# Optimization experiments

Hardware: AMD Instinct MI355X
Metric: run time of the kernel (lower is better)

## Reference

```python
import jax, jax.numpy as jnp
import numpy as np

B, CI, CO = 4, 64, 128
N_IN, N_OUT, K, P, H = 65536, 16384, 9, 4, 32
EPS = 1e-5


def setup_inputs() -> dict:
    key = jax.random.key(0)
    ks = jax.random.split(key, 16)
    inp = {
        "x": jax.random.normal(ks[0], (B, CI, N_IN), jnp.float32),
        "off1": jax.random.normal(ks[1], (N_OUT, K, 2), jnp.float32),
        "off2": jax.random.normal(ks[2], (N_OUT, K, 2), jnp.float32),
        "nbr1": jax.random.randint(ks[3], (N_OUT, K), 0, N_IN),
        "nbr2": jax.random.randint(ks[4], (N_OUT, K), 0, N_OUT),
        "pool_idx": jax.random.randint(ks[5], (N_OUT, P), 0, N_IN),
        # shared weight_net: 2 -> H -> 1 MLP producing per-neighbor interp weight
        "wn_w1": jax.random.normal(ks[6], (2, H), jnp.float32) * 0.5,
        "wn_b1": jnp.zeros((H,), jnp.float32),
        "wn_w2": jax.random.normal(ks[7], (H, 1), jnp.float32) * 0.5,
        "wn_b2": jnp.zeros((1,), jnp.float32),
        # conv weights [C_out, C_in, K]
        "W1": jax.random.normal(ks[8], (CO, CI, K), jnp.float32) * (1.0 / np.sqrt(CI * K)),
        "W2": jax.random.normal(ks[9], (CO, CO, K), jnp.float32) * (1.0 / np.sqrt(CO * K)),
        # batchnorm affine params
        "bn1_g": jnp.ones((CO,), jnp.float32),
        "bn1_b": jnp.zeros((CO,), jnp.float32),
        "bn2_g": jnp.ones((CO,), jnp.float32),
        "bn2_b": jnp.zeros((CO,), jnp.float32),
        # 1x1 expand conv
        "exp_w": jax.random.normal(ks[10], (CO, CI), jnp.float32) * (1.0 / np.sqrt(CI)),
        "exp_b": jnp.zeros((CO,), jnp.float32),
    }
    return inp


def _weight_net(off, w1, b1, w2, b2):
    # off: [M, K, 2] -> interp weights [M, K]
    h = jax.nn.relu(off @ w1 + b1)
    return (h @ w2 + b2)[..., 0]


def _interp_conv(x, W, idx, a):
    # x: [B, Ci, N_in], idx: [M, K], a: [M, K], W: [Co, Ci, K]
    g = x[:, :, idx]  # gather -> [B, Ci, M, K]
    return jnp.einsum("bimk,mk,oik->bom", g, a, W)


def _bn(x, g, b):
    # training-mode BatchNorm1d over (batch, points) per channel
    m = x.mean(axis=(0, 2), keepdims=True)
    v = x.var(axis=(0, 2), keepdims=True)
    return (x - m) * jax.lax.rsqrt(v + EPS) * g[None, :, None] + b[None, :, None]


def reference(x, off1, off2, wn_w1, wn_b1, wn_w2, wn_b2, W1, W2,
              bn1_g, bn1_b, bn2_g, bn2_b, exp_w, exp_b,
              nbr1, nbr2, pool_idx):
    a1 = _weight_net(off1, wn_w1, wn_b1, wn_w2, wn_b2)  # [M, K]
    out = _interp_conv(x, W1, nbr1, a1)                  # [B, Co, M]
    out = jax.nn.relu(_bn(out, bn1_g, bn1_b))
    a2 = _weight_net(off2, wn_w1, wn_b1, wn_w2, wn_b2)
    out = _interp_conv(out, W2, nbr2, a2)
    out = _bn(out, bn2_g, bn2_b)
    # downsample identity: AvgPoolNG over 4 nearest in_locs per out_loc
    identity = x[:, :, pool_idx].mean(axis=-1)           # [B, Ci, M]
    # expand channels: 1x1 conv
    identity = jnp.einsum("oi,bim->bom", exp_w, identity) + exp_b[None, :, None]
    return jax.nn.relu(out + identity)
```

## Files before the change

kernel.cpp:

```cpp
#include <hip/hip_runtime.h>
#include <hip/hip_bf16.h>

#define B_    4
#define CI_   64
#define CO_   128
#define NIN_  65536
#define NOUT_ 16384
#define KK_   9
#define PP_   4
#define HH_   32

typedef _Float16 f16x8 __attribute__((ext_vector_type(8)));
typedef _Float16 f16x4 __attribute__((ext_vector_type(4)));
typedef float    f32x4 __attribute__((ext_vector_type(4)));


__global__ void zero_kernel(float* p, int n) {
    int i = blockIdx.x * 256 + threadIdx.x;
    if (i < n) p[i] = 0.f;
}

__global__ void wnet_kernel(const float* __restrict__ off1, const float* __restrict__ off2,
                            const float* __restrict__ w1, const float* __restrict__ b1,
                            const float* __restrict__ w2, const float* __restrict__ b2,
                            float* __restrict__ a1, float* __restrict__ a2) {
    int idx = blockIdx.x * 256 + threadIdx.x;
    if (idx >= NOUT_ * KK_) return;
    float x0 = off1[idx*2+0], x1 = off1[idx*2+1];
    float y0 = off2[idx*2+0], y1 = off2[idx*2+1];
    float bias2 = b2[0];
    float s1 = bias2, s2 = bias2;
    #pragma unroll
    for (int h = 0; h < HH_; ++h) {
        float wh0 = w1[h], wh1 = w1[HH_+h], bh = b1[h], vh = w2[h];
        s1 += fmaxf(x0*wh0 + x1*wh1 + bh, 0.f) * vh;
        s2 += fmaxf(y0*wh0 + y1*wh1 + bh, 0.f) * vh;
    }
    a1[idx] = s1;
    a2[idx] = s2;
}

template<int CIN>
__global__ void wpack_kernel(const float* __restrict__ W, _Float16* __restrict__ Wf) {
    constexpr int NSLAB = (CIN/64) * KK_;
    int f = blockIdx.x * 256 + threadIdx.x;
    if (f >= NSLAB * 8192) return;
    int j   = f & 7;
    int l   = (f >> 3) & 63;
    int ot  = (f >> 9) & 7;
    int kap = (f >> 12) & 1;
    int s   = f >> 13;
    int o   = ot*16 + (l & 15);
    int kel = kap*32 + ((l >> 4) & 3)*8 + j;
    int k, i;
    if (CIN == 64) { k = s; i = kel; }
    else           { k = s >> 1; i = ((s & 1) << 6) + kel; }
    Wf[f] = (_Float16)W[((size_t)o*CIN + i)*KK_ + k];
}

__global__ void epack_kernel(const float* __restrict__ E, _Float16* __restrict__ Ef) {
    int f = blockIdx.x * 256 + threadIdx.x;
    if (f >= 8192) return;
    int j   = f & 7;
    int l   = (f >> 3) & 63;
    int ot  = (f >> 9) & 7;
    int kap = (f >> 12) & 1;
    int o   = ot*16 + (l & 15);
    int i   = kap*32 + ((l >> 4) & 3)*8 + j;
    Ef[f] = (_Float16)E[o*64 + i];
}

__global__ void xtrans_kernel(const float* __restrict__ x, _Float16* __restrict__ xT) {
    __shared__ float tile[64][65];
    int p0 = blockIdx.x * 64;
    int b  = blockIdx.y;
    int t  = threadIdx.x;
    #pragma unroll
    for (int r = 0; r < 16; ++r) {
        int f = r*256 + t;
        int i = f >> 6, pp = f & 63;
        tile[i][pp] = x[((size_t)(b*CI_ + i))*NIN_ + p0 + pp];
    }
    __syncthreads();
    #pragma unroll
    for (int r = 0; r < 2; ++r) {
        int f  = r*256 + t;
        int pp = f >> 3;
        int i0 = (f & 7) * 8;
        f16x8 v;
        #pragma unroll
        for (int e = 0; e < 8; ++e) v[e] = (_Float16)tile[i0+e][pp];
        *(f16x8*)(xT + ((size_t)(p0+pp)*B_ + b)*CI_ + i0) = v;
    }
}

__global__ __launch_bounds__(256) void bnreduce_kernel(const float* __restrict__ pbuf,
                                                       float* __restrict__ stats) {
    int t = threadIdx.x;
    float s = 0.f;
    int base = blockIdx.x * 32;
    #pragma unroll
    for (int b = 0; b < 32; ++b)
        s += pbuf[(size_t)(base + b)*256 + t];
    atomicAdd(&stats[t], s);
}

__global__ void bnparams_kernel(const float* __restrict__ gsum, const float* __restrict__ gsq,
                                const float* __restrict__ g, const float* __restrict__ bb,
                                const float* __restrict__ eb,
                                float* __restrict__ scbi) {
    int o = threadIdx.x;
    const float inv_n = 1.f / (B_ * NOUT_);
    float mean = gsum[o] * inv_n;
    float var  = gsq[o] * inv_n - mean*mean;
    float sc   = g[o] * rsqrtf(var + 1e-5f);
    scbi[o]       = sc;
    scbi[128 + o] = bb[o] - mean*sc + eb[o];
}

__global__ __launch_bounds__(256) void bnrelu_kernel(_Float16* __restrict__ t,
                                                     const float* __restrict__ scbi) {
    __shared__ float ssc[128], sbi[128];
    if (threadIdx.x < 128) {
        ssc[threadIdx.x] = scbi[threadIdx.x];
        sbi[threadIdx.x] = scbi[128 + threadIdx.x];
    }
    __syncthreads();
    size_t idx = ((size_t)blockIdx.x*256 + threadIdx.x) * 8;
    int o0 = (int)(idx & 127);
    f16x8 v = *(f16x8*)(t + idx);
    #pragma unroll
    for (int e = 0; e < 8; ++e) {
        float f = (float)v[e] * ssc[o0+e] + sbi[o0+e];
        v[e] = (_Float16)fmaxf(f, 0.f);
    }
    *(f16x8*)(t + idx) = v;
}

template<int CIN>
__global__ __launch_bounds__(256, CIN == 64 ? 4 : 3) void conv_mfma_kernel(
    const _Float16* __restrict__ in,
    const _Float16* __restrict__ Wf,
    const int*      __restrict__ nbr,
    const float*    __restrict__ amk,
    _Float16*       __restrict__ outh,
    float*          __restrict__ pbuf)
{
    constexpr int NKAP = CIN/32;
    __shared__ _Float16 Gs[2][64*CIN];
    const int t    = threadIdx.x;
    const int lane = t & 63;
    const int wid  = t >> 6;
    const int wr   = wid >> 1, wc = wid & 1;
    const int m0   = blockIdx.x * 16;
    const int l15 = lane & 15, l4 = lane >> 4, l7 = lane & 7;
    const int srow = t >> 2;
    const int sq   = t & 3;
    const int sb   = srow & 3;
    const int sm   = m0 + (srow >> 2);

    int   pn[KK_];
    float pa[KK_];
    #pragma unroll
    for (int k = 0; k < KK_; ++k) { pn[k] = nbr[sm*KK_ + k]; pa[k] = amk[sm*KK_ + k]; }

    f32x4 acc[4][2];
    #pragma unroll
    for (int c = 0; c < 4; ++c)
        #pragma unroll
        for (int j = 0; j < 2; ++j)
            acc[c][j] = (f32x4){0.f, 0.f, 0.f, 0.f};

    f16x8 greg[NKAP];
    {
        const _Float16* src = in + ((size_t)pn[0]*B_ + sb)*CIN + sq*(CIN/4);
        #pragma unroll
        for (int q = 0; q < NKAP; ++q) greg[q] = *(const f16x8*)(src + q*8);
    }

    #pragma unroll
    for (int s = 0; s < KK_; ++s) {
        const _Float16 hs = (_Float16)pa[s];
        #pragma unroll
        for (int q = 0; q < NKAP; ++q) {
            f16x8 v = greg[q];
            #pragma unroll
            for (int e = 0; e < 8; ++e) v[e] = v[e] * hs;
            const int c4 = sq*NKAP + q;
            *(f16x8*)(&Gs[s&1][srow*CIN + ((c4 ^ (srow & 7)) << 3)]) = v;
        }
        __syncthreads();
        f16x8 gn[NKAP];
        if (s + 1 < KK_) {
            const _Float16* src = in + ((size_t)pn[s+1]*B_ + sb)*CIN + sq*(CIN/4);
            #pragma unroll
            for (int q = 0; q < NKAP; ++q) gn[q] = *(const f16x8*)(src + q*8);
        }
        #pragma unroll
        for (int kap = 0; kap < NKAP; ++kap) {
            f16x8 aF[4], bF[2];
            const _Float16* wbase = Wf + ((size_t)(s*NKAP + kap)*8*64)*8;
            #pragma unroll
            for (int c = 0; c < 4; ++c)
                aF[c] = *(const f16x8*)(wbase + (((wr*4 + c)*64 + lane) << 3));
            #pragma unroll
            for (int jt = 0; jt < 2; ++jt) {
                const int row = wc*32 + jt*16 + l15;
                const int ch  = (kap*4 + l4) ^ l7;
                bF[jt] = *(const f16x8*)(&Gs[s&1][row*CIN + (ch << 3)]);
            }
            #pragma unroll
            for (int c = 0; c < 4; ++c)
                #pragma unroll
                for (int jt = 0; jt < 2; ++jt)
                    acc[c][jt] = __builtin_amdgcn_mfma_f32_16x16x32_f16(
                        aF[c], bF[jt], acc[c][jt], 0, 0, 0);
        }
        if (s + 1 < KK_) {
            #pragma unroll
            for (int q = 0; q < NKAP; ++q) greg[q] = gn[q];
        }
    }

    __syncthreads();
    float* red = (float*)Gs;
    #pragma unroll
    for (int c = 0; c < 4; ++c) {
        #pragma unroll
        for (int r = 0; r < 4; ++r) {
            float s = acc[c][0][r] + acc[c][1][r];
            float q = acc[c][0][r]*acc[c][0][r] + acc[c][1][r]*acc[c][1][r];
            #pragma unroll
            for (int msk = 1; msk <= 8; msk <<= 1) {
                s += __shfl_xor(s, msk);
                q += __shfl_xor(q, msk);
            }
            if (l15 == 0) {
                const int o = wr*64 + c*16 + l4*4 + r;
                red[wc*256 + o]       = s;
                red[wc*256 + 128 + o] = q;
            }
        }
    }
    __syncthreads();
    pbuf[(size_t)blockIdx.x*256 + t] = red[t] + red[256 + t];
    #pragma unroll
    for (int c = 0; c < 4; ++c) {
        const int o = wr*64 + c*16 + l4*4;
        #pragma unroll
        for (int jt = 0; jt < 2; ++jt) {
            const int n = wc*32 + jt*16 + l15;
            f16x4 h;
            #pragma unroll
            for (int r = 0; r < 4; ++r) h[r] = (_Float16)acc[c][jt][r];
            *(f16x4*)(outh + ((size_t)(m0*B_) + n)*CO_ + o) = h;
        }
    }
}

__global__ __launch_bounds__(256, 4) void final_mfma_kernel(
    const _Float16* __restrict__ xh,
    const _Float16* __restrict__ out2T,
    const int*      __restrict__ pool_idx,
    const _Float16* __restrict__ Ef,
    const float*    __restrict__ scbi2,
    float*          __restrict__ out)
{
    __shared__ _Float16 Gs[64*64];
    const int t    = threadIdx.x;
    const int lane = t & 63;
    const int wid  = t >> 6;
    const int wr   = wid >> 1, wc = wid & 1;
    const int m0   = blockIdx.x * 16;
    const int l15 = lane & 15, l4 = lane >> 4, l7 = lane & 7;

    {
        const int srow = t >> 2;
        const int sq   = t & 3;
        const int m    = m0 + (srow & 15);
        const int b    = srow >> 4;
        const int4 pidx = *(const int4*)(pool_idx + m*4);
        const _Float16* r0 = xh + ((size_t)pidx.x*B_ + b)*CI_ + sq*16;
        const _Float16* r1 = xh + ((size_t)pidx.y*B_ + b)*CI_ + sq*16;
        const _Float16* r2 = xh + ((size_t)pidx.z*B_ + b)*CI_ + sq*16;
        const _Float16* r3 = xh + ((size_t)pidx.w*B_ + b)*CI_ + sq*16;
        #pragma unroll
        for (int q = 0; q < 2; ++q) {
            f16x8 v  = *(const f16x8*)(r0 + q*8);
            f16x8 v1 = *(const f16x8*)(r1 + q*8);
            f16x8 v2 = *(const f16x8*)(r2 + q*8);
            f16x8 v3 = *(const f16x8*)(r3 + q*8);
            v = v + v1 + v2 + v3;
            #pragma unroll
            for (int e = 0; e < 8; ++e) v[e] = v[e] * (_Float16)0.25f;
            const int c4 = sq*2 + q;
            *(f16x8*)(Gs + srow*64 + ((c4 ^ (srow & 7)) << 3)) = v;
        }
    }
    __syncthreads();

    f32x4 acc[4][2];
    #pragma unroll
    for (int c = 0; c < 4; ++c)
        #pragma unroll
        for (int j = 0; j < 2; ++j)
            acc[c][j] = (f32x4){0.f, 0.f, 0.f, 0.f};
    #pragma unroll
    for (int kap = 0; kap < 2; ++kap) {
        f16x8 aF[4], bF[2];
        #pragma unroll
        for (int c = 0; c < 4; ++c)
            aF[c] = *(const f16x8*)(Ef + ((size_t)((kap*8 + wr*4 + c)*64 + lane))*8);
        #pragma unroll
        for (int jt = 0; jt < 2; ++jt) {
            const int row = wc*32 + jt*16 + l15;
            const int ch  = (kap*4 + l4) ^ l7;
            bF[jt] = *(const f16x8*)(Gs + row*64 + (ch << 3));
        }
        #pragma unroll
        for (int c = 0; c < 4; ++c)
            #pragma unroll
            for (int jt = 0; jt < 2; ++jt)
                acc[c][jt] = __builtin_amdgcn_mfma_f32_16x16x32_f16(
                    aF[c], bF[jt], acc[c][jt], 0, 0, 0);
    }

    const int m = m0 + l15;
    #pragma unroll
    for (int c = 0; c < 4; ++c) {
        const int o = wr*64 + c*16 + l4*4;
        const float4 sc4 = *(const float4*)(scbi2 + o);
        const float4 bi4 = *(const float4*)(scbi2 + 128 + o);
        #pragma unroll
        for (int jt = 0; jt < 2; ++jt) {
            const int b = wc*2 + jt;
            const f16x4 v2 = *(const f16x4*)(out2T + ((size_t)(m*B_ + b))*CO_ + o);
            float res0 = fmaxf(acc[c][jt][0] + (float)v2[0]*sc4.x + bi4.x, 0.f);
            float res1 = fmaxf(acc[c][jt][1] + (float)v2[1]*sc4.y + bi4.y, 0.f);
            float res2 = fmaxf(acc[c][jt][2] + (float)v2[2]*sc4.z + bi4.z, 0.f);
            float res3 = fmaxf(acc[c][jt][3] + (float)v2[3]*sc4.w + bi4.w, 0.f);
            out[((size_t)(b*CO_ + o + 0))*NOUT_ + m] = res0;
            out[((size_t)(b*CO_ + o + 1))*NOUT_ + m] = res1;
            out[((size_t)(b*CO_ + o + 2))*NOUT_ + m] = res2;
            out[((size_t)(b*CO_ + o + 3))*NOUT_ + m] = res3;
        }
    }
}

extern "C" void kernel_launch(void* const* d_in, const int* in_sizes, int n_in,
                              void* d_out, int out_size, void* d_ws, size_t ws_size,
                              hipStream_t stream) {
    const float* x        = (const float*)d_in[0];
    const float* off1     = (const float*)d_in[1];
    const float* off2     = (const float*)d_in[2];
    const int*   nbr1     = (const int*)  d_in[3];
    const int*   nbr2     = (const int*)  d_in[4];
    const int*   pool_idx = (const int*)  d_in[5];
    const float* wn_w1    = (const float*)d_in[6];
    const float* wn_b1    = (const float*)d_in[7];
    const float* wn_w2    = (const float*)d_in[8];
    const float* wn_b2    = (const float*)d_in[9];
    const float* W1       = (const float*)d_in[10];
    const float* W2       = (const float*)d_in[11];
    const float* bn1_g    = (const float*)d_in[12];
    const float* bn1_b    = (const float*)d_in[13];
    const float* bn2_g    = (const float*)d_in[14];
    const float* bn2_b    = (const float*)d_in[15];
    const float* exp_w    = (const float*)d_in[16];
    const float* exp_b    = (const float*)d_in[17];
    float* out = (float*)d_out;

    char* ws = (char*)d_ws;
    float* a1      = (float*)ws;  ws += (size_t)NOUT_*KK_*4;
    float* a2      = (float*)ws;  ws += (size_t)NOUT_*KK_*4;
    float* scbi1   = (float*)ws;  ws += 256*4;
    float* scbi2   = (float*)ws;  ws += 256*4;
    float* stats   = (float*)ws;  ws += 640*4;
    float* pbuf    = (float*)ws;  ws += (size_t)1024*256*4;
    _Float16* Wf1  = (_Float16*)ws; ws += (size_t)9*8192*2;
    _Float16* Wf2  = (_Float16*)ws; ws += (size_t)18*8192*2;
    _Float16* Ef   = (_Float16*)ws; ws += (size_t)8192*2;
    _Float16* xh   = (_Float16*)ws; ws += (size_t)NIN_*B_*CI_*2;
    _Float16* o1h  = (_Float16*)ws; ws += (size_t)NOUT_*B_*CO_*2;
    _Float16* o2h  = (_Float16*)ws; ws += (size_t)NOUT_*B_*CO_*2;

    float* sum1  = stats;       float* sq1 = stats + 128;
    float* sum2  = stats + 256; float* sq2 = stats + 384;
    float* fzero = stats + 512;

    zero_kernel<<<3, 256, 0, stream>>>(stats, 640);
    wnet_kernel<<<(NOUT_*KK_ + 255)/256, 256, 0, stream>>>(off1, off2, wn_w1, wn_b1, wn_w2, wn_b2, a1, a2);
    wpack_kernel<CI_><<<(9*8192 + 255)/256, 256, 0, stream>>>(W1, Wf1);
    wpack_kernel<CO_><<<(18*8192 + 255)/256, 256, 0, stream>>>(W2, Wf2);
    epack_kernel<<<32, 256, 0, stream>>>(exp_w, Ef);
    xtrans_kernel<<<dim3(NIN_/64, B_), 256, 0, stream>>>(x, xh);

    conv_mfma_kernel<CI_><<<NOUT_/16, 256, 0, stream>>>(xh, Wf1, nbr1, a1, o1h, pbuf);
    bnreduce_kernel<<<32, 256, 0, stream>>>(pbuf, sum1);
    bnparams_kernel<<<1, 128, 0, stream>>>(sum1, sq1, bn1_g, bn1_b, fzero, scbi1);
    bnrelu_kernel<<<4096, 256, 0, stream>>>(o1h, scbi1);

    conv_mfma_kernel<CO_><<<NOUT_/16, 256, 0, stream>>>(o1h, Wf2, nbr2, a2, o2h, pbuf);
    bnreduce_kernel<<<32, 256, 0, stream>>>(pbuf, sum2);
    bnparams_kernel<<<1, 128, 0, stream>>>(sum2, sq2, bn2_g, bn2_b, exp_b, scbi2);

    final_mfma_kernel<<<NOUT_/16, 256, 0, stream>>>(xh, o2h, pool_idx, Ef, scbi2, out);
}
```

Baseline: 132.6 us.

## Load conv B-fragments directly from global, dropping LDS staging and barriers

```diff
diff --git a/kernel.cpp b/kernel.cpp
--- a/kernel.cpp
+++ b/kernel.cpp
@@ -138,7 +138,7 @@
 }
 
 template<int CIN>
-__global__ __launch_bounds__(256, CIN == 64 ? 4 : 3) void conv_mfma_kernel(
+__global__ __launch_bounds__(256, 4) void conv_mfma_kernel(
     const _Float16* __restrict__ in,
     const _Float16* __restrict__ Wf,
     const int*      __restrict__ nbr,
@@ -147,22 +147,24 @@
     float*          __restrict__ pbuf)
 {
     constexpr int NKAP = CIN/32;
-    __shared__ _Float16 Gs[2][64*CIN];
+    constexpr int NST  = KK_ * NKAP;
+    __shared__ float red[512];
     const int t    = threadIdx.x;
     const int lane = t & 63;
     const int wid  = t >> 6;
     const int wr   = wid >> 1, wc = wid & 1;
+    const int wc2  = wc*2;
     const int m0   = blockIdx.x * 16;
-    const int l15 = lane & 15, l4 = lane >> 4, l7 = lane & 7;
-    const int srow = t >> 2;
-    const int sq   = t & 3;
-    const int sb   = srow & 3;
-    const int sm   = m0 + (srow >> 2);
-
-    int   pn[KK_];
-    float pa[KK_];
-    #pragma unroll
-    for (int k = 0; k < KK_; ++k) { pn[k] = nbr[sm*KK_ + k]; pa[k] = amk[sm*KK_ + k]; }
+    const int l15  = lane & 15, l4 = lane >> 4;
+
+    const int sm = m0 + l15;
+    int      pn[KK_];
+    _Float16 pa[KK_];
+    #pragma unroll
+    for (int k = 0; k < KK_; ++k) {
+        pn[k] = nbr[sm*KK_ + k];
+        pa[k] = (_Float16)amk[sm*KK_ + k];
+    }
 
     f32x4 acc[4][2];
     #pragma unroll
@@ -171,59 +173,40 @@
         for (int j = 0; j < 2; ++j)
             acc[c][j] = (f32x4){0.f, 0.f, 0.f, 0.f};
 
-    f16x8 greg[NKAP];
+    f16x8 bfr[2][2], afr[2][4];
     {
-        const _Float16* src = in + ((size_t)pn[0]*B_ + sb)*CIN + sq*(CIN/4);
-        #pragma unroll
-        for (int q = 0; q < NKAP; ++q) greg[q] = *(const f16x8*)(src + q*8);
-    }
-
-    #pragma unroll
-    for (int s = 0; s < KK_; ++s) {
-        const _Float16 hs = (_Float16)pa[s];
-        #pragma unroll
-        for (int q = 0; q < NKAP; ++q) {
-            f16x8 v = greg[q];
-            #pragma unroll
-            for (int e = 0; e < 8; ++e) v[e] = v[e] * hs;
-            const int c4 = sq*NKAP + q;
-            *(f16x8*)(&Gs[s&1][srow*CIN + ((c4 ^ (srow & 7)) << 3)]) = v;
-        }
-        __syncthreads();
-        f16x8 gn[NKAP];
-        if (s + 1 < KK_) {
-            const _Float16* src = in + ((size_t)pn[s+1]*B_ + sb)*CIN + sq*(CIN/4);
-            #pragma unroll
-            for (int q = 0; q < NKAP; ++q) gn[q] = *(const f16x8*)(src + q*8);
-        }
-        #pragma unroll
-        for (int kap = 0; kap < NKAP; ++kap) {
-            f16x8 aF[4], bF[2];
-            const _Float16* wbase = Wf + ((size_t)(s*NKAP + kap)*8*64)*8;
-            #pragma unroll
-            for (int c = 0; c < 4; ++c)
-                aF[c] = *(const f16x8*)(wbase + (((wr*4 + c)*64 + lane) << 3));
-            #pragma unroll
-            for (int jt = 0; jt < 2; ++jt) {
-                const int row = wc*32 + jt*16 + l15;
-                const int ch  = (kap*4 + l4) ^ l7;
-                bF[jt] = *(const f16x8*)(&Gs[s&1][row*CIN + (ch << 3)]);
-            }
-            #pragma unroll
-            for (int c = 0; c < 4; ++c)
-                #pragma unroll
-                for (int jt = 0; jt < 2; ++jt)
-                    acc[c][jt] = __builtin_amdgcn_mfma_f32_16x16x32_f16(
-                        aF[c], bF[jt], acc[c][jt], 0, 0, 0);
-        }
-        if (s + 1 < KK_) {
-            #pragma unroll
-            for (int q = 0; q < NKAP; ++q) greg[q] = gn[q];
-        }
-    }
-
-    __syncthreads();
-    float* red = (float*)Gs;
+        const _Float16* bsrc = in + ((size_t)pn[0]*B_ + wc2)*CIN + l4*8;
+        bfr[0][0] = *(const f16x8*)bsrc;
+        bfr[0][1] = *(const f16x8*)(bsrc + CIN);
+        const _Float16* wsrc = Wf + (size_t)(wr*4)*512 + lane*8;
+        #pragma unroll
+        for (int c = 0; c < 4; ++c) afr[0][c] = *(const f16x8*)(wsrc + c*512);
+    }
+
+    #pragma unroll
+    for (int st = 0; st < NST; ++st) {
+        const int cur = st & 1, nxt = cur ^ 1;
+        if (st + 1 < NST) {
+            const int s2 = (st+1) / NKAP, kap2 = (st+1) % NKAP;
+            const _Float16* bsrc = in + ((size_t)pn[s2]*B_ + wc2)*CIN + kap2*32 + l4*8;
+            bfr[nxt][0] = *(const f16x8*)bsrc;
+            bfr[nxt][1] = *(const f16x8*)(bsrc + CIN);
+            const _Float16* wsrc = Wf + ((size_t)((s2*NKAP + kap2)*8 + wr*4))*512 + lane*8;
+            #pragma unroll
+            for (int c = 0; c < 4; ++c) afr[nxt][c] = *(const f16x8*)(wsrc + c*512);
+        }
+        const int s = st / NKAP;
+        const _Float16 hs = pa[s];
+        f16x8 b0 = bfr[cur][0], b1 = bfr[cur][1];
+        #pragma unroll
+        for (int e = 0; e < 8; ++e) { b0[e] *= hs; b1[e] *= hs; }
+        #pragma unroll
+        for (int c = 0; c < 4; ++c) {
+            acc[c][0] = __builtin_amdgcn_mfma_f32_16x16x32_f16(afr[cur][c], b0, acc[c][0], 0, 0, 0);
+            acc[c][1] = __builtin_amdgcn_mfma_f32_16x16x32_f16(afr[cur][c], b1, acc[c][1], 0, 0, 0);
+        }
+    }
+
     #pragma unroll
     for (int c = 0; c < 4; ++c) {
         #pragma unroll
@@ -244,16 +227,17 @@
     }
     __syncthreads();
     pbuf[(size_t)blockIdx.x*256 + t] = red[t] + red[256 + t];
+
     #pragma unroll
     for (int c = 0; c < 4; ++c) {
         const int o = wr*64 + c*16 + l4*4;
         #pragma unroll
         for (int jt = 0; jt < 2; ++jt) {
-            const int n = wc*32 + jt*16 + l15;
+            const size_t row = (size_t)(m0 + l15)*B_ + wc2 + jt;
             f16x4 h;
             #pragma unroll
             for (int r = 0; r < 4; ++r) h[r] = (_Float16)acc[c][jt][r];
-            *(f16x4*)(outh + ((size_t)(m0*B_) + n)*CO_ + o) = h;
+            *(f16x4*)(outh + row*CO_ + o) = h;
         }
     }
 }
```

New measurement: 159.0 us. 19.9% more time.
